# Kernel tuning notes

Hardware: AMD Instinct MI355X
Metric: run time of the kernel (lower is better)

Reference implementation:

```python
import jax, jax.numpy as jnp
import numpy as np
import math

B, QLEN, KLEN = 8, 128, 1024
KDIM = QDIM = ADIM = ODIM = 512
HM, HC = 4, 4            # monotonic / chunkwise heads
CHUNK = 4                # chunkwise attention window
EPS = 1e-6
SHARPENING = 1.0
NEG_INF = float(np.finfo(np.float32).min)


def moving_sum(x, back, forward):
    """Windowed sum over last axis: out[k] = sum_{j=k-back}^{k+forward} x[j].
    Equivalent to the conv1d-with-ones-filter moving_sum in the torch code."""
    K = x.shape[-1]
    xp = jnp.pad(x, [(0, 0)] * (x.ndim - 1) + [(back, forward)])
    cs = jnp.cumsum(xp, axis=-1)
    L = back + forward + 1
    upper = jax.lax.slice_in_dim(cs, L - 1, L - 1 + K, axis=-1)
    lower = jnp.concatenate([jnp.zeros_like(cs[..., :1]),
                             jax.lax.slice_in_dim(cs, 0, K - 1, axis=-1)], axis=-1)
    return upper - lower


def safe_cumprod(x, eps):
    """exp(exclusive_cumsum(log(clip(x, eps, 1)))) along last axis."""
    logx = jnp.log(jnp.clip(x, eps, 1.0))
    excl = jnp.concatenate([jnp.zeros_like(logx[..., :1]),
                            jnp.cumsum(logx, axis=-1)[..., :-1]], axis=-1)
    return jnp.exp(excl)


def _heads(x, w, b, h):
    y = x @ w + b                                   # [B, L, ADIM]
    bs, L, _ = y.shape
    return y.reshape(bs, L, h, -1).transpose(0, 2, 1, 3)  # [B, h, L, d_k]


def setup_inputs() -> dict:
    key = jax.random.key(0)
    ks = jax.random.split(key, 16)
    s = 0.02
    f32 = jnp.float32
    return {
        "key_x": jax.random.normal(ks[0], (B, KLEN, KDIM), f32),
        "query_x": jax.random.normal(ks[1], (B, QLEN, QDIM), f32),
        "mask": jnp.ones((B, QLEN, KLEN), jnp.int32),
        "wk_m": jax.random.normal(ks[2], (KDIM, ADIM), f32) * s,
        "bk_m": jnp.zeros((ADIM,), f32),
        "wq_m": jax.random.normal(ks[3], (QDIM, ADIM), f32) * s,
        "bq_m": jnp.zeros((ADIM,), f32),
        "r": jnp.asarray(-4.0, f32),
        "wk_c": jax.random.normal(ks[4], (KDIM, ADIM), f32) * s,
        "bk_c": jnp.zeros((ADIM,), f32),
        "wq_c": jax.random.normal(ks[5], (QDIM, ADIM), f32) * s,
        "bq_c": jnp.zeros((ADIM,), f32),
        "wv": jax.random.normal(ks[6], (KDIM, ADIM), f32) * s,
        "bv": jnp.zeros((ADIM,), f32),
        "wo": jax.random.normal(ks[7], (ADIM, ODIM), f32) * s,
        "bo": jnp.zeros((ODIM,), f32),
    }


def reference(key_x, query_x, mask, wk_m, bk_m, wq_m, bq_m, r,
              wk_c, bk_c, wq_c, bq_c, wv, bv, wo, bo):
    scale = math.sqrt(ADIM)
    m = (mask[:, None] > 0)                                    # [B,1,Q,K]

    # ---- monotonic energy (scaled_dot + offset r) ----
    km = _heads(key_x, wk_m, bk_m, HM)                         # [B,HM,K,dk]
    qm = _heads(query_x, wq_m, bq_m, HM)                       # [B,HM,Q,dk]
    e_mono = jnp.einsum('bhqd,bhkd->bhqk', qm, km) / scale + r
    e_mono = jnp.where(m, e_mono, NEG_INF)

    # ---- monotonic alpha via safe_cumprod + per-step cumsum recurrence ----
    p_choose = jax.nn.sigmoid(e_mono)                          # [B,HM,Q,K]
    cp = safe_cumprod(1.0 - p_choose, EPS)                     # [B,HM,Q,K]
    aw0 = jnp.zeros((B, HM, KLEN), e_mono.dtype).at[..., 0].set(1.0)

    def step(aw_prev, pc):
        p_i, cp_i = pc                                         # [B,HM,K]
        aw = p_i * cp_i * jnp.cumsum(aw_prev / jnp.maximum(cp_i, EPS), axis=-1)
        return aw, aw

    _, alpha = jax.lax.scan(step, aw0,
                            (p_choose.transpose(2, 0, 1, 3),
                             cp.transpose(2, 0, 1, 3)))
    alpha = alpha.transpose(1, 2, 0, 3)                        # [B,HM,Q,K]

    # ---- chunkwise energy ----
    kc = _heads(key_x, wk_c, bk_c, HC)
    qc = _heads(query_x, wq_c, bq_c, HC)
    e_chunk = jnp.einsum('bhqd,bhkd->bhqk', qc, kc) / scale
    e_chunk = jnp.where(m, e_chunk, NEG_INF)

    # ---- efficient chunkwise attention (clipped-logit trick) ----
    e = e_chunk - jnp.max(e_chunk, axis=-1, keepdims=True)
    sexp = jnp.maximum(jnp.exp(e), 1e-5)[:, None]              # [B,1,HC,Q,K]
    denom = moving_sum(sexp, CHUNK - 1, 0)                     # [B,1,HC,Q,K]
    beta = sexp * moving_sum(alpha[:, :, None] * SHARPENING / denom,
                             0, CHUNK - 1)                     # [B,HM,HC,Q,K]
    beta = beta.reshape(B, HM * HC, QLEN, KLEN)

    # ---- context + output projection ----
    v = (key_x @ wv + bv).reshape(B, KLEN, HM * HC, ADIM // (HM * HC))
    cv = jnp.einsum('bhqk,bkhd->bqhd', beta, v).reshape(B, QLEN, ADIM)
    return cv @ wo + bo
```

## Files before the change

kernel.cpp:

```cpp
#include <hip/hip_runtime.h>
#include <hip/hip_bf16.h>


#define NEG_INF (-3.402823466e38f)
#define EPS_MOCHA 1e-6f
#define INV_SCALE 0.04419417382415922f

typedef _Float16 half8 __attribute__((ext_vector_type(8)));
typedef _Float16 half4v __attribute__((ext_vector_type(4)));
typedef float f32x4 __attribute__((ext_vector_type(4)));

#define WAITBAR(N) asm volatile("s_waitcnt vmcnt(" #N ") lgkmcnt(0)\n\ts_barrier" ::: "memory")

__device__ __forceinline__ float wave_incl_scan(float x)
{
    int v;
    v = __builtin_amdgcn_update_dpp(0, __builtin_bit_cast(int, x), 0x111, 0xF, 0xF, false);
    x += __builtin_bit_cast(float, v);
    v = __builtin_amdgcn_update_dpp(0, __builtin_bit_cast(int, x), 0x112, 0xF, 0xF, false);
    x += __builtin_bit_cast(float, v);
    v = __builtin_amdgcn_update_dpp(0, __builtin_bit_cast(int, x), 0x114, 0xF, 0xF, false);
    x += __builtin_bit_cast(float, v);
    v = __builtin_amdgcn_update_dpp(0, __builtin_bit_cast(int, x), 0x118, 0xF, 0xF, false);
    x += __builtin_bit_cast(float, v);
    v = __builtin_amdgcn_update_dpp(0, __builtin_bit_cast(int, x), 0x142, 0xA, 0xF, false);
    x += __builtin_bit_cast(float, v);
    v = __builtin_amdgcn_update_dpp(0, __builtin_bit_cast(int, x), 0x143, 0xC, 0xF, false);
    x += __builtin_bit_cast(float, v);
    return x;
}

__global__ __launch_bounds__(256) void prep_weights(
    const float* __restrict__ wk_m, const float* __restrict__ wk_c,
    const float* __restrict__ wv, const float* __restrict__ wq_m,
    const float* __restrict__ wq_c, const float* __restrict__ wo,
    _Float16* __restrict__ Wt5, _Float16* __restrict__ Wt_wo)
{
    __shared__ float T[64][65];
    const int z = blockIdx.z;
    const float* W = (z == 0) ? wk_m : (z == 1) ? wk_c : (z == 2) ? wv
                   : (z == 3) ? wq_m : (z == 4) ? wq_c : wo;
    _Float16* O = (z < 5) ? (Wt5 + (size_t)z * 262144) : Wt_wo;
    const int n0 = blockIdx.x * 64, k0 = blockIdx.y * 64;
    const int t = threadIdx.x;
    const int rr = t >> 4, cc = (t & 15) * 4;
#pragma unroll
    for (int r = 0; r < 4; ++r) {
        int k = r * 16 + rr;
        float4 v = *(const float4*)(W + (size_t)(k0 + k) * 512 + n0 + cc);
        T[k][cc + 0] = v.x; T[k][cc + 1] = v.y;
        T[k][cc + 2] = v.z; T[k][cc + 3] = v.w;
    }
    __syncthreads();
    const int nn = t >> 2, kc = (t & 3) * 16;
    _Float16 tmp[16];
#pragma unroll
    for (int i = 0; i < 16; ++i) tmp[i] = (_Float16)T[kc + i][nn];
    _Float16* Op = O + (size_t)(n0 + nn) * 512 + k0 + kc;
    *(half8*)(Op)     = *(half8*)&tmp[0];
    *(half8*)(Op + 8) = *(half8*)&tmp[8];
}

__device__ __forceinline__ void mfma_step(half8 a[4], half8 b[4], f32x4 acc[4][4])
{
#pragma unroll
    for (int mt = 0; mt < 4; ++mt)
#pragma unroll
        for (int nt = 0; nt < 4; ++nt)
            acc[mt][nt] = __builtin_amdgcn_mfma_f32_16x16x32_f16(
                a[mt], b[nt], acc[mt][nt], 0, 0, 0);
}

__device__ __forceinline__ void stage16(const _Float16* src, _Float16* dst)
{
    __builtin_amdgcn_global_load_lds(
        (const __attribute__((address_space(1))) void*)src,
        (__attribute__((address_space(3))) void*)dst, 16, 0, 0);
}

__device__ __forceinline__ half8 cvt8(float4 a, float4 b)
{
    half8 h = {(_Float16)a.x, (_Float16)a.y, (_Float16)a.z, (_Float16)a.w,
               (_Float16)b.x, (_Float16)b.y, (_Float16)b.z, (_Float16)b.w};
    return h;
}

template <int NSTEPS>
__device__ __forceinline__ void gemm_acc_af32(
    const float* __restrict__ Abase, const _Float16* __restrict__ Bbase,
    _Float16* As, _Float16* Bs, f32x4 acc[4][4])
{
    const int tid = threadIdx.x;
    const int lane = tid & 63, wave = tid >> 6;
    const int wm = wave >> 1, wn = wave & 1;
    const int col = lane & 15, quad = lane >> 4;
    const int r0 = tid >> 2, seg = tid & 3;

    const float* Af0 = Abase + (size_t)r0 * 512 + seg * 8;
    const float* Af1 = Af0 + (size_t)64 * 512;
    const _Float16* Bg0 = Bbase + (size_t)r0 * 512 + seg * 8;
    const _Float16* Bg1 = Bg0 + (size_t)64 * 512;

    float4 pa0[2], pa1[2], pb0[2], pb1[2];

    pa0[0] = *(const float4*)(Af0);
    pa1[0] = *(const float4*)(Af0 + 4);
    pb0[0] = *(const float4*)(Af1);
    pb1[0] = *(const float4*)(Af1 + 4);
    stage16(Bg0, Bs + tid * 8);
    stage16(Bg1, Bs + 2048 + tid * 8);
    if (NSTEPS > 1) {
        stage16(Bg0 + 32, Bs + 4096 + tid * 8);
        stage16(Bg1 + 32, Bs + 4096 + 2048 + tid * 8);
    }
    *(half8*)(As + tid * 8)        = cvt8(pa0[0], pa1[0]);
    *(half8*)(As + 2048 + tid * 8) = cvt8(pb0[0], pb1[0]);
    if (NSTEPS > 1) {
        pa0[1] = *(const float4*)(Af0 + 32);
        pa1[1] = *(const float4*)(Af0 + 36);
        pb0[1] = *(const float4*)(Af1 + 32);
        pb1[1] = *(const float4*)(Af1 + 36);
    }
    if (NSTEPS > 1) WAITBAR(6);
    else            WAITBAR(0);

#pragma unroll
    for (int ks = 0; ks < NSTEPS; ++ks) {
        const int s = ks & 1;
        if (ks + 2 < NSTEPS) {
            const int k0 = (ks + 2) * 32;
            pa0[s] = *(const float4*)(Af0 + k0);
            pa1[s] = *(const float4*)(Af0 + k0 + 4);
            pb0[s] = *(const float4*)(Af1 + k0);
            pb1[s] = *(const float4*)(Af1 + k0 + 4);
        }
        if (ks + 2 < NSTEPS) {
            _Float16* Bbuf = Bs + ((ks + 2) % 3) * 4096;
            stage16(Bg0 + (ks + 2) * 32, Bbuf + tid * 8);
            stage16(Bg1 + (ks + 2) * 32, Bbuf + 2048 + tid * 8);
        }
        const _Float16* Afr = As + (ks & 1) * 4096 + (size_t)(wm * 64 + col) * 32 + quad * 8;
        const _Float16* Bfr = Bs + (ks % 3) * 4096 + (size_t)(wn * 64 + col) * 32 + quad * 8;
        half8 a[4], b[4];
#pragma unroll
        for (int t = 0; t < 4; ++t) {
            a[t] = *(const half8*)(Afr + (size_t)t * 16 * 32);
            b[t] = *(const half8*)(Bfr + (size_t)t * 16 * 32);
        }
        mfma_step(a, b, acc);
        if (ks + 1 < NSTEPS) {
            _Float16* Abuf = As + ((ks + 1) & 1) * 4096;
            *(half8*)(Abuf + tid * 8)        = cvt8(pa0[s ^ 1], pa1[s ^ 1]);
            *(half8*)(Abuf + 2048 + tid * 8) = cvt8(pb0[s ^ 1], pb1[s ^ 1]);
        }
        if (ks + 2 < NSTEPS)      WAITBAR(6);
        else if (ks + 1 < NSTEPS) WAITBAR(0);
    }
}

template <int NSTEPS>
__device__ __forceinline__ void gemm_acc_f16(
    const _Float16* __restrict__ Abase, const _Float16* __restrict__ Bbase,
    _Float16* As, _Float16* Bs, f32x4 acc[4][4])
{
    const int tid = threadIdx.x;
    const int lane = tid & 63, wave = tid >> 6;
    const int wm = wave >> 1, wn = wave & 1;
    const int col = lane & 15, quad = lane >> 4;
    const int r0 = tid >> 2, seg = tid & 3;

    const _Float16* Ag0 = Abase + (size_t)r0 * 512 + seg * 8;
    const _Float16* Ag1 = Ag0 + (size_t)64 * 512;
    const _Float16* Bg0 = Bbase + (size_t)r0 * 512 + seg * 8;
    const _Float16* Bg1 = Bg0 + (size_t)64 * 512;

    stage16(Ag0, As + tid * 8);
    stage16(Ag1, As + 2048 + tid * 8);
    stage16(Bg0, Bs + tid * 8);
    stage16(Bg1, Bs + 2048 + tid * 8);
    if (NSTEPS > 1) {
        stage16(Ag0 + 32, As + 4096 + tid * 8);
        stage16(Ag1 + 32, As + 4096 + 2048 + tid * 8);
        stage16(Bg0 + 32, Bs + 4096 + tid * 8);
        stage16(Bg1 + 32, Bs + 4096 + 2048 + tid * 8);
        WAITBAR(4);
    } else {
        WAITBAR(0);
    }

#pragma unroll
    for (int ks = 0; ks < NSTEPS; ++ks) {
        const int cur = ks % 3;
        if (ks + 2 < NSTEPS) {
            const int s2 = (ks + 2) % 3;
            stage16(Ag0 + (ks + 2) * 32, As + s2 * 4096 + tid * 8);
            stage16(Ag1 + (ks + 2) * 32, As + s2 * 4096 + 2048 + tid * 8);
            stage16(Bg0 + (ks + 2) * 32, Bs + s2 * 4096 + tid * 8);
            stage16(Bg1 + (ks + 2) * 32, Bs + s2 * 4096 + 2048 + tid * 8);
        }
        const _Float16* Afr = As + cur * 4096 + (size_t)(wm * 64 + col) * 32 + quad * 8;
        const _Float16* Bfr = Bs + cur * 4096 + (size_t)(wn * 64 + col) * 32 + quad * 8;
        half8 a[4], b[4];
#pragma unroll
        for (int t = 0; t < 4; ++t) {
            a[t] = *(const half8*)(Afr + (size_t)t * 16 * 32);
            b[t] = *(const half8*)(Bfr + (size_t)t * 16 * 32);
        }
        mfma_step(a, b, acc);
        if (ks + 2 < NSTEPS)      WAITBAR(4);
        else if (ks + 1 < NSTEPS) WAITBAR(0);
    }
}

__device__ __forceinline__ void proj_epilogue(
    f32x4 acc[4][4], const float* __restrict__ bias, void* __restrict__ Cv,
    int m0, int n0, int f16o)
{
    const int tid = threadIdx.x;
    const int lane = tid & 63, wave = tid >> 6;
    const int wm = wave >> 1, wn = wave & 1;
    const int col = lane & 15, quad = lane >> 4;
    float bnt[4];
#pragma unroll
    for (int nt = 0; nt < 4; ++nt)
        bnt[nt] = bias[n0 + wn * 64 + nt * 16 + col];
#pragma unroll
    for (int mt = 0; mt < 4; ++mt) {
        const int rowb = m0 + wm * 64 + mt * 16 + quad * 4;
#pragma unroll
        for (int nt = 0; nt < 4; ++nt) {
            const int cc = n0 + wn * 64 + nt * 16 + col;
#pragma unroll
            for (int r = 0; r < 4; ++r) {
                float v = acc[mt][nt][r] + bnt[nt];
                if (f16o)
                    ((_Float16*)Cv)[(size_t)(rowb + r) * 512 + cc] = (_Float16)v;
                else
                    ((float*)Cv)[(size_t)(rowb + r) * 512 + cc] = v;
            }
        }
    }
}

__global__ __launch_bounds__(256) void mfma_proj5(
    const float* __restrict__ key_x, const float* __restrict__ query_x,
    const _Float16* __restrict__ Wt5,
    const float* __restrict__ b0, void* __restrict__ C0,
    const float* __restrict__ b1, void* __restrict__ C1,
    const float* __restrict__ b2, void* __restrict__ C2,
    const float* __restrict__ b3, void* __restrict__ C3,
    const float* __restrict__ b4, void* __restrict__ C4)
{
    __shared__ _Float16 As[8192];
    __shared__ _Float16 Bs[12288];
    const int bid = (blockIdx.x & 7) * 104 + (blockIdx.x >> 3);
    int g, mblk, nblk;
    if (bid < 768) {
        g = bid >> 8; mblk = (bid & 255) >> 2; nblk = bid & 3;
    } else {
        const int t = bid - 768;
        g = 3 + (t >> 5); mblk = (t & 31) >> 2; nblk = t & 3;
    }
    const bool qry = g >= 3;
    const float* A = qry ? query_x : key_x;
    const _Float16* Wt = Wt5 + (size_t)g * 262144;
    const float* bias = (g == 0) ? b0 : (g == 1) ? b1 : (g == 2) ? b2
                      : (g == 3) ? b3 : b4;
    void* Cv = (g == 0) ? C0 : (g == 1) ? C1 : (g == 2) ? C2
             : (g == 3) ? C3 : C4;
    const int f16o = (g == 2) ? 0 : 1;
    const int m0 = mblk * 128, n0 = nblk * 128;

    f32x4 acc[4][4];
#pragma unroll
    for (int mt = 0; mt < 4; ++mt)
#pragma unroll
        for (int nt = 0; nt < 4; ++nt) acc[mt][nt] = (f32x4)0.f;
    gemm_acc_af32<16>(A + (size_t)m0 * 512, Wt + (size_t)n0 * 512, As, Bs, acc);
    proj_epilogue(acc, bias, Cv, m0, n0, f16o);
}

__global__ __launch_bounds__(256) void mfma_proj_out(
    const _Float16* __restrict__ A16, const _Float16* __restrict__ Wt,
    const float* __restrict__ bias, float* __restrict__ C)
{
    __shared__ _Float16 As[12288];
    __shared__ _Float16 Bs[12288];
    const int m0 = blockIdx.x * 128, n0 = blockIdx.y * 128;
    f32x4 acc[4][4];
#pragma unroll
    for (int mt = 0; mt < 4; ++mt)
#pragma unroll
        for (int nt = 0; nt < 4; ++nt) acc[mt][nt] = (f32x4)0.f;
    gemm_acc_f16<16>(A16 + (size_t)m0 * 512, Wt + (size_t)n0 * 512, As, Bs, acc);
    proj_epilogue(acc, bias, C, m0, n0, 0);
}

__global__ __launch_bounds__(256) void energy_mfma(
    const _Float16* __restrict__ Qm, const _Float16* __restrict__ Km,
    const _Float16* __restrict__ Qc, const _Float16* __restrict__ Kc,
    const int* __restrict__ mask, float* __restrict__ e_mono,
    _Float16* __restrict__ e_chunk16, const float* __restrict__ r_ptr)
{
    __shared__ _Float16 As[12288];
    __shared__ _Float16 Bs[12288];
    const int tid = threadIdx.x;
    const int lane = tid & 63, wave = tid >> 6;
    const int wm = wave >> 1, wn = wave & 1;
    const int col = lane & 15, quad = lane >> 4;
    const int kt0 = blockIdx.x * 128;
    const int h = blockIdx.y;
    const int b = blockIdx.z;
    const float rv = r_ptr[0];
    const int r0 = tid >> 2, seg = tid & 3;

    const _Float16* QmB = Qm + (size_t)(b * 128) * 512 + h * 128;
    const _Float16* QcB = Qc + (size_t)(b * 128) * 512 + h * 128;
    const _Float16* KmB = Km + (size_t)(b * 1024 + kt0) * 512 + h * 128;
    const _Float16* KcB = Kc + (size_t)(b * 1024 + kt0) * 512 + h * 128;
    const _Float16* Am0 = QmB + (size_t)r0 * 512 + seg * 8;
    const _Float16* Ac0 = QcB + (size_t)r0 * 512 + seg * 8;
    const _Float16* Bm0 = KmB + (size_t)r0 * 512 + seg * 8;
    const _Float16* Bc0 = KcB + (size_t)r0 * 512 + seg * 8;
#define EGA(s) (((s) < 4 ? Am0 : Ac0) + ((s) & 3) * 32)
#define EGB(s) (((s) < 4 ? Bm0 : Bc0) + ((s) & 3) * 32)

    f32x4 accM[4][4], accC[4][4];
#pragma unroll
    for (int mt = 0; mt < 4; ++mt)
#pragma unroll
        for (int nt = 0; nt < 4; ++nt) { accM[mt][nt] = (f32x4)0.f; accC[mt][nt] = (f32x4)0.f; }

#pragma unroll
    for (int s = 0; s < 2; ++s) {
        stage16(EGA(s), As + s * 4096 + tid * 8);
        stage16(EGA(s) + (size_t)64 * 512, As + s * 4096 + 2048 + tid * 8);
        stage16(EGB(s), Bs + s * 4096 + tid * 8);
        stage16(EGB(s) + (size_t)64 * 512, Bs + s * 4096 + 2048 + tid * 8);
    }
    WAITBAR(4);

#pragma unroll
    for (int ks = 0; ks < 8; ++ks) {
        const int cur = ks % 3;
        if (ks + 2 < 8) {
            const int s2 = (ks + 2) % 3;
            stage16(EGA(ks + 2), As + s2 * 4096 + tid * 8);
            stage16(EGA(ks + 2) + (size_t)64 * 512, As + s2 * 4096 + 2048 + tid * 8);
            stage16(EGB(ks + 2), Bs + s2 * 4096 + tid * 8);
            stage16(EGB(ks + 2) + (size_t)64 * 512, Bs + s2 * 4096 + 2048 + tid * 8);
        }
        const _Float16* Afr = As + cur * 4096 + (size_t)(wm * 64 + col) * 32 + quad * 8;
        const _Float16* Bfr = Bs + cur * 4096 + (size_t)(wn * 64 + col) * 32 + quad * 8;
        half8 a[4], bfr[4];
#pragma unroll
        for (int t = 0; t < 4; ++t) {
            a[t]   = *(const half8*)(Afr + (size_t)t * 16 * 32);
            bfr[t] = *(const half8*)(Bfr + (size_t)t * 16 * 32);
        }
        if (ks < 4) mfma_step(a, bfr, accM);
        else        mfma_step(a, bfr, accC);
        if (ks + 2 < 8)      WAITBAR(4);
        else if (ks + 1 < 8) WAITBAR(0);
    }
#undef EGA
#undef EGB

#pragma unroll
    for (int mt = 0; mt < 4; ++mt) {
        const int qb = wm * 64 + mt * 16 + quad * 4;
#pragma unroll
        for (int nt = 0; nt < 4; ++nt) {
            const int kc = kt0 + wn * 64 + nt * 16 + col;
#pragma unroll
            for (int r = 0; r < 4; ++r) {
                const int q = qb + r;
                const int mv = mask[((size_t)b * 128 + q) * 1024 + kc];
                const size_t oi = (((size_t)b * 4 + h) * 128 + q) * 1024 + kc;
                float vm = accM[mt][nt][r] * INV_SCALE + rv;
                e_mono[oi] = mv ? vm : NEG_INF;
                float vc = accC[mt][nt][r] * INV_SCALE;
                e_chunk16[oi] = (_Float16)(mv ? vc : NEG_INF);
            }
        }
    }
}

__device__ __forceinline__ void transcend_row(
    const float* __restrict__ Erow, int lane, float o_pcp[16], float o_inv[16])
{
    const float* E = Erow + lane * 16;
    float e[16];
    *(float4*)&e[0]  = *(const float4*)(E);
    *(float4*)&e[4]  = *(const float4*)(E + 4);
    *(float4*)&e[8]  = *(const float4*)(E + 8);
    *(float4*)&e[12] = *(const float4*)(E + 12);

    float p[16], l[16];
#pragma unroll
    for (int i = 0; i < 16; ++i) {
        p[i] = 1.f / (1.f + expf(-e[i]));
        l[i] = logf(fmaxf(1.f - p[i], EPS_MOCHA));
    }
    float incl[16];
    incl[0] = l[0];
#pragma unroll
    for (int i = 1; i < 16; ++i) incl[i] = incl[i - 1] + l[i];
    float total = incl[15];
    float x = wave_incl_scan(total);
    float base = x - total;
#pragma unroll
    for (int i = 0; i < 16; ++i) {
        float cl = base + (i ? incl[i - 1] : 0.f);
        float cp = expf(cl);
        o_pcp[i] = p[i] * cp;
        o_inv[i] = 1.f / fmaxf(cp, EPS_MOCHA);
    }
}

#define SW2(k) ((k) + ((k) >> 4))

__global__ __launch_bounds__(256) void alpha_pre(
    const float* __restrict__ e_mono, float* __restrict__ G,
    float* __restrict__ pcp)
{
    __shared__ float pshare[4][1088];
    const int tid = threadIdx.x;
    const int lane = tid & 63;
    const int wid = tid >> 6;
    const int row = blockIdx.x * 4 + wid;
    const int q = row & 127;

    float pq[16], iq[16];
    transcend_row(e_mono + (size_t)row * 1024, lane, pq, iq);

    float* P = pcp + (size_t)row * 1024 + lane * 16;
    *(float4*)(P)      = *(float4*)&pq[0];
    *(float4*)(P + 4)  = *(float4*)&pq[4];
    *(float4*)(P + 8)  = *(float4*)&pq[8];
    *(float4*)(P + 12) = *(float4*)&pq[12];

#pragma unroll
    for (int i = 0; i < 16; ++i)
        pshare[wid][SW2(lane * 16 + i)] = pq[i];
    __syncthreads();

    float g[16];
    if (q == 0) {
#pragma unroll
        for (int i = 0; i < 16; ++i) g[i] = 0.f;
        if (lane == 0) g[0] = iq[0];
    } else if (wid > 0) {
#pragma unroll
        for (int i = 0; i < 16; ++i)
            g[i] = pshare[wid - 1][SW2(lane * 16 + i)] * iq[i];
    } else {
        float pm[16], im[16];
        transcend_row(e_mono + (size_t)(row - 1) * 1024, lane, pm, im);
#pragma unroll
        for (int i = 0; i < 16; ++i) g[i] = pm[i] * iq[i];
    }
    float* Gp = G + (size_t)row * 1024 + lane * 16;
    *(float4*)(Gp)      = *(float4*)&g[0];
    *(float4*)(Gp + 4)  = *(float4*)&g[4];
    *(float4*)(Gp + 8)  = *(float4*)&g[8];
    *(float4*)(Gp + 12) = *(float4*)&g[12];
}

__global__ __launch_bounds__(64, 1) void alpha_scan(
    const float* __restrict__ G, float* __restrict__ S)
{
    const int lane = threadIdx.x;
    const int bh = blockIdx.x;
    const float* Gp = G + (size_t)bh * 131072 + lane * 16;
    float* Sp = S + (size_t)bh * 131072 + lane * 16;

    float bg[8][16];
#pragma unroll
    for (int s = 0; s < 8; ++s) {
        const float* Gq = Gp + (size_t)s * 1024;
        *(float4*)&bg[s][0]  = *(const float4*)(Gq);
        *(float4*)&bg[s][4]  = *(const float4*)(Gq + 4);
        *(float4*)&bg[s][8]  = *(const float4*)(Gq + 8);
        *(float4*)&bg[s][12] = *(const float4*)(Gq + 12);
    }

    float Sv[16];
#pragma unroll
    for (int i = 0; i < 16; ++i) Sv[i] = 1.f;

    for (int q8 = 0; q8 < 128; q8 += 8) {
#pragma unroll
        for (int s = 0; s < 8; ++s) {
            const int q = q8 + s;
            float g[16];
#pragma unroll
            for (int i = 0; i < 16; ++i) g[i] = bg[s][i];
            if (q + 8 < 128) {
                const float* Gq = Gp + (size_t)(q + 8) * 1024;
                *(float4*)&bg[s][0]  = *(const float4*)(Gq);
                *(float4*)&bg[s][4]  = *(const float4*)(Gq + 4);
                *(float4*)&bg[s][8]  = *(const float4*)(Gq + 8);
                *(float4*)&bg[s][12] = *(const float4*)(Gq + 12);
            }

            float incl[16];
            incl[0] = g[0] * Sv[0];
#pragma unroll
            for (int i = 1; i < 16; ++i)
                incl[i] = fmaf(g[i], Sv[i], incl[i - 1]);
            float total = incl[15];
            float x = wave_incl_scan(total);
            float base = x - total;
#pragma unroll
            for (int i = 0; i < 16; ++i) Sv[i] = base + incl[i];

            float* Sq = Sp + (size_t)q * 1024;
            *(float4*)(Sq)      = *(float4*)&Sv[0];
            *(float4*)(Sq + 4)  = *(float4*)&Sv[4];
            *(float4*)(Sq + 8)  = *(float4*)&Sv[8];
            *(float4*)(Sq + 12) = *(float4*)&Sv[12];
        }
    }
}

__global__ __launch_bounds__(256) void beta_kernel(
    const _Float16* __restrict__ e_chunk16, const float* __restrict__ pcp,
    const float* __restrict__ S, _Float16* __restrict__ beta)
{
    __shared__ float red[4];
    __shared__ float edge_sx[4][4];
    __shared__ float edge_t[4][4][4];
    const int q = blockIdx.x, b = blockIdx.y;
    const int tid = threadIdx.x;
    const int lane = tid & 63, wid = tid >> 6;
    const int k4 = tid * 4;

    float av[4][4];
#pragma unroll
    for (int hm = 0; hm < 4; ++hm) {
        const size_t off = (((size_t)b * 4 + hm) * 128 + q) * 1024 + k4;
        float4 pv = *(const float4*)(pcp + off);
        float4 sv = *(const float4*)(S + off);
        av[hm][0] = pv.x * sv.x;
        av[hm][1] = pv.y * sv.y;
        av[hm][2] = pv.z * sv.z;
        av[hm][3] = pv.w * sv.w;
    }

    for (int hc = 0; hc < 4; ++hc) {
        half4v ev = *(const half4v*)(e_chunk16 + (((size_t)b * 4 + hc) * 128 + q) * 1024 + k4);
        float e[4] = {(float)ev[0], (float)ev[1], (float)ev[2], (float)ev[3]};

        float mx = fmaxf(fmaxf(e[0], e[1]), fmaxf(e[2], e[3]));
#pragma unroll
        for (int off = 32; off >= 1; off >>= 1)
            mx = fmaxf(mx, __shfl_xor(mx, off, 64));
        if (lane == 0) red[wid] = mx;
        __syncthreads();
        mx = fmaxf(fmaxf(red[0], red[1]), fmaxf(red[2], red[3]));

        float sx[4];
#pragma unroll
        for (int i = 0; i < 4; ++i)
            sx[i] = fmaxf(expf(e[i] - mx), 1e-5f);
        if (lane == 63) {
            edge_sx[wid][0] = sx[0]; edge_sx[wid][1] = sx[1];
            edge_sx[wid][2] = sx[2]; edge_sx[wid][3] = sx[3];
        }
        __syncthreads();

        float p1 = __shfl_up(sx[3], 1, 64);
        float p2 = __shfl_up(sx[2], 1, 64);
        float p3 = __shfl_up(sx[1], 1, 64);
        if (lane == 0) {
            if (wid > 0) {
                p1 = edge_sx[wid - 1][3];
                p2 = edge_sx[wid - 1][2];
                p3 = edge_sx[wid - 1][1];
            } else {
                p1 = 0.f; p2 = 0.f; p3 = 0.f;
            }
        }
        float den[4];
        den[0] = sx[0] + p1 + p2 + p3;
        den[1] = sx[1] + sx[0] + p1 + p2;
        den[2] = sx[2] + sx[1] + sx[0] + p1;
        den[3] = sx[3] + sx[2] + sx[1] + sx[0];

        float t[4][4];
#pragma unroll
        for (int hm = 0; hm < 4; ++hm)
#pragma unroll
            for (int i = 0; i < 4; ++i)
                t[hm][i] = av[hm][i] / den[i];
        if (lane == 0) {
#pragma unroll
            for (int hm = 0; hm < 4; ++hm) {
                edge_t[wid][hm][0] = t[hm][0]; edge_t[wid][hm][1] = t[hm][1];
                edge_t[wid][hm][2] = t[hm][2]; edge_t[wid][hm][3] = t[hm][3];
            }
        }
        __syncthreads();

#pragma unroll
        for (int hm = 0; hm < 4; ++hm) {
            float n1 = __shfl_down(t[hm][0], 1, 64);
            float n2 = __shfl_down(t[hm][1], 1, 64);
            float n3 = __shfl_down(t[hm][2], 1, 64);
            if (lane == 63) {
                if (wid < 3) {
                    n1 = edge_t[wid + 1][hm][0];
                    n2 = edge_t[wid + 1][hm][1];
                    n3 = edge_t[wid + 1][hm][2];
                } else {
                    n1 = 0.f; n2 = 0.f; n3 = 0.f;
                }
            }
            float o0 = sx[0] * (t[hm][0] + t[hm][1] + t[hm][2] + t[hm][3]);
            float o1 = sx[1] * (t[hm][1] + t[hm][2] + t[hm][3] + n1);
            float o2 = sx[2] * (t[hm][2] + t[hm][3] + n1 + n2);
            float o3 = sx[3] * (t[hm][3] + n1 + n2 + n3);
            _Float16* Brow = beta + (((size_t)b * 16 + hm * 4 + hc) * 128 + q) * 1024;
            half4v hv = {(_Float16)o0, (_Float16)o1, (_Float16)o2, (_Float16)o3};
            *(half4v*)(Brow + k4) = hv;
        }
    }
}

__global__ __launch_bounds__(256) void context_kernel(
    const _Float16* __restrict__ beta, const float* __restrict__ V,
    _Float16* __restrict__ cv16)
{
    __shared__ float bS[128][64];
    __shared__ float vS[128][32];
    const int qh = blockIdx.x, h = blockIdx.y, b = blockIdx.z;
    const int tid = threadIdx.x;
    const int ty = tid >> 3, tx = tid & 7;
    const int q0 = qh * 64;

    const _Float16* Bbase = beta + (((size_t)b * 16 + h) * 128 + q0) * 1024;
    const float* Vbase = V + (size_t)b * 1024 * 512 + h * 32;

    float acc[2][4];
#pragma unroll
    for (int i = 0; i < 2; ++i)
#pragma unroll
        for (int j = 0; j < 4; ++j) acc[i][j] = 0.f;

    for (int k0 = 0; k0 < 1024; k0 += 128) {
        {
            int r = tid >> 2, c = tid & 3;
#pragma unroll
            for (int s = 0; s < 4; ++s) {
                half8 v = *(const half8*)(Bbase + (size_t)r * 1024 + k0 + s * 32 + c * 8);
#pragma unroll
                for (int j = 0; j < 8; ++j) bS[s * 32 + c * 8 + j][r] = (float)v[j];
            }
        }
        {
            int kk = tid >> 3, c = tid & 7;
#pragma unroll
            for (int s = 0; s < 4; ++s) {
                float4 v = *(const float4*)(Vbase + (size_t)(k0 + s * 32 + kk) * 512 + c * 4);
                *(float4*)&vS[s * 32 + kk][c * 4] = v;
            }
        }
        __syncthreads();
#pragma unroll 8
        for (int kk = 0; kk < 128; ++kk) {
            float a0 = bS[kk][ty * 2], a1 = bS[kk][ty * 2 + 1];
            float bb[4];
            *(float4*)bb = *(const float4*)&vS[kk][tx * 4];
#pragma unroll
            for (int j = 0; j < 4; ++j) {
                acc[0][j] = fmaf(a0, bb[j], acc[0][j]);
                acc[1][j] = fmaf(a1, bb[j], acc[1][j]);
            }
        }
        __syncthreads();
    }
#pragma unroll
    for (int i = 0; i < 2; ++i) {
        _Float16* Cp = cv16 + ((size_t)b * 128 + q0 + ty * 2 + i) * 512 + h * 32 + tx * 4;
        half4v hv = {(_Float16)acc[i][0], (_Float16)acc[i][1],
                     (_Float16)acc[i][2], (_Float16)acc[i][3]};
        *(half4v*)Cp = hv;
    }
}

extern "C" void kernel_launch(void* const* d_in, const int* in_sizes, int n_in,
                              void* d_out, int out_size, void* d_ws, size_t ws_size,
                              hipStream_t stream)
{
    const float* key_x   = (const float*)d_in[0];
    const float* query_x = (const float*)d_in[1];
    const int*   mask    = (const int*)d_in[2];
    const float* wk_m = (const float*)d_in[3];
    const float* bk_m = (const float*)d_in[4];
    const float* wq_m = (const float*)d_in[5];
    const float* bq_m = (const float*)d_in[6];
    const float* r    = (const float*)d_in[7];
    const float* wk_c = (const float*)d_in[8];
    const float* bk_c = (const float*)d_in[9];
    const float* wq_c = (const float*)d_in[10];
    const float* bq_c = (const float*)d_in[11];
    const float* wv   = (const float*)d_in[12];
    const float* bv   = (const float*)d_in[13];
    const float* wo   = (const float*)d_in[14];
    const float* bo   = (const float*)d_in[15];
    float* out = (float*)d_out;

    float* ws = (float*)d_ws;
    _Float16* hws = (_Float16*)d_ws;
    const size_t MEGF = 1024 * 1024;
    _Float16* Km16  = hws;
    _Float16* Kc16  = hws + 4 * MEGF;
    _Float16* Qm16  = hws + 8 * MEGF;
    _Float16* Qc16  = hws + 8 * MEGF + 524288;
    float* e_mono  = ws + 11 * MEGF;
    _Float16* e_chunk16 = hws + 34 * MEGF;
    float* V       = ws + 19 * MEGF;
    float* G       = ws;
    float* pcp     = ws + 4 * MEGF;
    float* S       = ws + 23 * MEGF;
    _Float16* beta16 = hws + 16 * MEGF;
    _Float16* Wt5   = hws + 54 * MEGF;
    _Float16* Wt_wo = hws + 54 * MEGF + 5 * 262144;
    _Float16* cv16  = hws + 55 * MEGF + MEGF / 2;

    prep_weights<<<dim3(8, 8, 6), 256, 0, stream>>>(
        wk_m, wk_c, wv, wq_m, wq_c, wo, Wt5, Wt_wo);
    mfma_proj5<<<dim3(832), 256, 0, stream>>>(
        key_x, query_x, Wt5,
        bk_m, Km16, bk_c, Kc16, bv, V, bq_m, Qm16, bq_c, Qc16);
    energy_mfma<<<dim3(8, 4, 8), 256, 0, stream>>>(
        Qm16, Km16, Qc16, Kc16, mask, e_mono, e_chunk16, r);
    alpha_pre<<<dim3(1024), 256, 0, stream>>>(e_mono, G, pcp);
    alpha_scan<<<dim3(32), 64, 0, stream>>>(G, S);
    beta_kernel<<<dim3(128, 8), 256, 0, stream>>>(e_chunk16, pcp, S, beta16);
    context_kernel<<<dim3(2, 16, 8), 256, 0, stream>>>(beta16, V, cv16);
    mfma_proj_out<<<dim3(8, 4), 256, 0, stream>>>(cv16, Wt_wo, bo, out);
}
```

Before: 256.8 us.

## Pre-convert activations to fp16 and use 512-thread 8-wave GEMM blocks

Adds a separate kernel that converts key_x and query_x to fp16 up front, so the projection GEMM can stage both operands through direct global-to-LDS loads. The projection, energy and output GEMMs move from 256-thread blocks (4 waves, 4x4 MFMA tiles each) to 512-thread blocks (8 waves, 4x2 tiles each). This halves per-wave accumulator registers and raises wave count per block to improve latency hiding. It costs an extra kernel launch plus a full fp16 write and re-read of the activations, and each wave now does less work per LDS fragment load.

```diff
diff --git a/kernel.cpp b/kernel.cpp
--- a/kernel.cpp
+++ b/kernel.cpp
@@ -30,6 +30,25 @@
     return x;
 }
 
+__device__ __forceinline__ half8 cvt8(float4 a, float4 b)
+{
+    half8 h = {(_Float16)a.x, (_Float16)a.y, (_Float16)a.z, (_Float16)a.w,
+               (_Float16)b.x, (_Float16)b.y, (_Float16)b.z, (_Float16)b.w};
+    return h;
+}
+
+__global__ __launch_bounds__(256) void cvt_x(
+    const float* __restrict__ key_x, const float* __restrict__ query_x,
+    _Float16* __restrict__ X16)
+{
+    const size_t KELEMS = (size_t)8192 * 512;
+    size_t o = ((size_t)blockIdx.x * 256 + threadIdx.x) * 8;
+    const float* s = (o < KELEMS) ? (key_x + o) : (query_x + (o - KELEMS));
+    float4 a = *(const float4*)s;
+    float4 b = *(const float4*)(s + 4);
+    *(half8*)(X16 + o) = cvt8(a, b);
+}
+
 __global__ __launch_bounds__(256) void prep_weights(
     const float* __restrict__ wk_m, const float* __restrict__ wk_c,
     const float* __restrict__ wv, const float* __restrict__ wq_m,
@@ -61,16 +80,6 @@
     *(half8*)(Op + 8) = *(half8*)&tmp[8];
 }
 
-__device__ __forceinline__ void mfma_step(half8 a[4], half8 b[4], f32x4 acc[4][4])
-{
-#pragma unroll
-    for (int mt = 0; mt < 4; ++mt)
-#pragma unroll
-        for (int nt = 0; nt < 4; ++nt)
-            acc[mt][nt] = __builtin_amdgcn_mfma_f32_16x16x32_f16(
-                a[mt], b[nt], acc[mt][nt], 0, 0, 0);
-}
-
 __device__ __forceinline__ void stage16(const _Float16* src, _Float16* dst)
 {
     __builtin_amdgcn_global_load_lds(
@@ -78,112 +87,26 @@
         (__attribute__((address_space(3))) void*)dst, 16, 0, 0);
 }
 
-__device__ __forceinline__ half8 cvt8(float4 a, float4 b)
-{
-    half8 h = {(_Float16)a.x, (_Float16)a.y, (_Float16)a.z, (_Float16)a.w,
-               (_Float16)b.x, (_Float16)b.y, (_Float16)b.z, (_Float16)b.w};
-    return h;
-}
-
 template <int NSTEPS>
-__device__ __forceinline__ void gemm_acc_af32(
-    const float* __restrict__ Abase, const _Float16* __restrict__ Bbase,
-    _Float16* As, _Float16* Bs, f32x4 acc[4][4])
+__device__ __forceinline__ void gemm8_f16(
+    const _Float16* __restrict__ Abase, const _Float16* __restrict__ Bbase,
+    _Float16* As, _Float16* Bs, f32x4 acc[4][2])
 {
     const int tid = threadIdx.x;
     const int lane = tid & 63, wave = tid >> 6;
-    const int wm = wave >> 1, wn = wave & 1;
+    const int wm = wave >> 2, wn = wave & 3;
     const int col = lane & 15, quad = lane >> 4;
     const int r0 = tid >> 2, seg = tid & 3;
 
-    const float* Af0 = Abase + (size_t)r0 * 512 + seg * 8;
-    const float* Af1 = Af0 + (size_t)64 * 512;
-    const _Float16* Bg0 = Bbase + (size_t)r0 * 512 + seg * 8;
-    const _Float16* Bg1 = Bg0 + (size_t)64 * 512;
-
-    float4 pa0[2], pa1[2], pb0[2], pb1[2];
-
-    pa0[0] = *(const float4*)(Af0);
-    pa1[0] = *(const float4*)(Af0 + 4);
-    pb0[0] = *(const float4*)(Af1);
-    pb1[0] = *(const float4*)(Af1 + 4);
-    stage16(Bg0, Bs + tid * 8);
-    stage16(Bg1, Bs + 2048 + tid * 8);
+    const _Float16* Ag = Abase + (size_t)r0 * 512 + seg * 8;
+    const _Float16* Bg = Bbase + (size_t)r0 * 512 + seg * 8;
+
+    stage16(Ag, As + tid * 8);
+    stage16(Bg, Bs + tid * 8);
     if (NSTEPS > 1) {
-        stage16(Bg0 + 32, Bs + 4096 + tid * 8);
-        stage16(Bg1 + 32, Bs + 4096 + 2048 + tid * 8);
-    }
-    *(half8*)(As + tid * 8)        = cvt8(pa0[0], pa1[0]);
-    *(half8*)(As + 2048 + tid * 8) = cvt8(pb0[0], pb1[0]);
-    if (NSTEPS > 1) {
-        pa0[1] = *(const float4*)(Af0 + 32);
-        pa1[1] = *(const float4*)(Af0 + 36);
-        pb0[1] = *(const float4*)(Af1 + 32);
-        pb1[1] = *(const float4*)(Af1 + 36);
-    }
-    if (NSTEPS > 1) WAITBAR(6);
-    else            WAITBAR(0);
-
-#pragma unroll
-    for (int ks = 0; ks < NSTEPS; ++ks) {
-        const int s = ks & 1;
-        if (ks + 2 < NSTEPS) {
-            const int k0 = (ks + 2) * 32;
-            pa0[s] = *(const float4*)(Af0 + k0);
-            pa1[s] = *(const float4*)(Af0 + k0 + 4);
-            pb0[s] = *(const float4*)(Af1 + k0);
-            pb1[s] = *(const float4*)(Af1 + k0 + 4);
-        }
-        if (ks + 2 < NSTEPS) {
-            _Float16* Bbuf = Bs + ((ks + 2) % 3) * 4096;
-            stage16(Bg0 + (ks + 2) * 32, Bbuf + tid * 8);
-            stage16(Bg1 + (ks + 2) * 32, Bbuf + 2048 + tid * 8);
-        }
-        const _Float16* Afr = As + (ks & 1) * 4096 + (size_t)(wm * 64 + col) * 32 + quad * 8;
-        const _Float16* Bfr = Bs + (ks % 3) * 4096 + (size_t)(wn * 64 + col) * 32 + quad * 8;
-        half8 a[4], b[4];
-#pragma unroll
-        for (int t = 0; t < 4; ++t) {
-            a[t] = *(const half8*)(Afr + (size_t)t * 16 * 32);
-            b[t] = *(const half8*)(Bfr + (size_t)t * 16 * 32);
-        }
-        mfma_step(a, b, acc);
-        if (ks + 1 < NSTEPS) {
-            _Float16* Abuf = As + ((ks + 1) & 1) * 4096;
-            *(half8*)(Abuf + tid * 8)        = cvt8(pa0[s ^ 1], pa1[s ^ 1]);
-            *(half8*)(Abuf + 2048 + tid * 8) = cvt8(pb0[s ^ 1], pb1[s ^ 1]);
-        }
-        if (ks + 2 < NSTEPS)      WAITBAR(6);
-        else if (ks + 1 < NSTEPS) WAITBAR(0);
-    }
-}
-
-template <int NSTEPS>
-__device__ __forceinline__ void gemm_acc_f16(
-    const _Float16* __restrict__ Abase, const _Float16* __restrict__ Bbase,
-    _Float16* As, _Float16* Bs, f32x4 acc[4][4])
-{
-    const int tid = threadIdx.x;
-    const int lane = tid & 63, wave = tid >> 6;
-    const int wm = wave >> 1, wn = wave & 1;
-    const int col = lane & 15, quad = lane >> 4;
-    const int r0 = tid >> 2, seg = tid & 3;
-
-    const _Float16* Ag0 = Abase + (size_t)r0 * 512 + seg * 8;
-    const _Float16* Ag1 = Ag0 + (size_t)64 * 512;
-    const _Float16* Bg0 = Bbase + (size_t)r0 * 512 + seg * 8;
-    const _Float16* Bg1 = Bg0 + (size_t)64 * 512;
-
-    stage16(Ag0, As + tid * 8);
-    stage16(Ag1, As + 2048 + tid * 8);
-    stage16(Bg0, Bs + tid * 8);
-    stage16(Bg1, Bs + 2048 + tid * 8);
-    if (NSTEPS > 1) {
-        stage16(Ag0 + 32, As + 4096 + tid * 8);
-        stage16(Ag1 + 32, As + 4096 + 2048 + tid * 8);
-        stage16(Bg0 + 32, Bs + 4096 + tid * 8);
-        stage16(Bg1 + 32, Bs + 4096 + 2048 + tid * 8);
-        WAITBAR(4);
+        stage16(Ag + 32, As + 4096 + tid * 8);
+        stage16(Bg + 32, Bs + 4096 + tid * 8);
+        WAITBAR(2);
     } else {
         WAITBAR(0);
     }
@@ -193,43 +116,45 @@
         const int cur = ks % 3;
         if (ks + 2 < NSTEPS) {
             const int s2 = (ks + 2) % 3;
-            stage16(Ag0 + (ks + 2) * 32, As + s2 * 4096 + tid * 8);
-            stage16(Ag1 + (ks + 2) * 32, As + s2 * 4096 + 2048 + tid * 8);
-            stage16(Bg0 + (ks + 2) * 32, Bs + s2 * 4096 + tid * 8);
-            stage16(Bg1 + (ks + 2) * 32, Bs + s2 * 4096 + 2048 + tid * 8);
+            stage16(Ag + (ks + 2) * 32, As + s2 * 4096 + tid * 8);
+            stage16(Bg + (ks + 2) * 32, Bs + s2 * 4096 + tid * 8);
         }
         const _Float16* Afr = As + cur * 4096 + (size_t)(wm * 64 + col) * 32 + quad * 8;
-        const _Float16* Bfr = Bs + cur * 4096 + (size_t)(wn * 64 + col) * 32 + quad * 8;
-        half8 a[4], b[4];
-#pragma unroll
-        for (int t = 0; t < 4; ++t) {
-            a[t] = *(const half8*)(Afr + (size_t)t * 16 * 32);
-            b[t] = *(const half8*)(Bfr + (size_t)t * 16 * 32);
-        }
-        mfma_step(a, b, acc);
-        if (ks + 2 < NSTEPS)      WAITBAR(4);
+        const _Float16* Bfr = Bs + cur * 4096 + (size_t)(wn * 32 + col) * 32 + quad * 8;
+        half8 a[4], b[2];
+#pragma unroll
+        for (int t = 0; t < 4; ++t) a[t] = *(const half8*)(Afr + (size_t)t * 16 * 32);
+#pragma unroll
+        for (int t = 0; t < 2; ++t) b[t] = *(const half8*)(Bfr + (size_t)t * 16 * 32);
+#pragma unroll
+        for (int mt = 0; mt < 4; ++mt)
+#pragma unroll
+            for (int nt = 0; nt < 2; ++nt)
+                acc[mt][nt] = __builtin_amdgcn_mfma_f32_16x16x32_f16(
+                    a[mt], b[nt], acc[mt][nt], 0, 0, 0);
+        if (ks + 2 < NSTEPS)      WAITBAR(2);
         else if (ks + 1 < NSTEPS) WAITBAR(0);
     }
 }
 
-__device__ __forceinline__ void proj_epilogue(
-    f32x4 acc[4][4], const float* __restrict__ bias, void* __restrict__ Cv,
+__device__ __forceinline__ void proj_epilogue8(
+    f32x4 acc[4][2], const float* __restrict__ bias, void* __restrict__ Cv,
     int m0, int n0, int f16o)
 {
     const int tid = threadIdx.x;
     const int lane = tid & 63, wave = tid >> 6;
-    const int wm = wave >> 1, wn = wave & 1;
+    const int wm = wave >> 2, wn = wave & 3;
     const int col = lane & 15, quad = lane >> 4;
-    float bnt[4];
-#pragma unroll
-    for (int nt = 0; nt < 4; ++nt)
-        bnt[nt] = bias[n0 + wn * 64 + nt * 16 + col];
+    float bnt[2];
+#pragma unroll
+    for (int nt = 0; nt < 2; ++nt)
+        bnt[nt] = bias[n0 + wn * 32 + nt * 16 + col];
 #pragma unroll
     for (int mt = 0; mt < 4; ++mt) {
         const int rowb = m0 + wm * 64 + mt * 16 + quad * 4;
 #pragma unroll
-        for (int nt = 0; nt < 4; ++nt) {
-            const int cc = n0 + wn * 64 + nt * 16 + col;
+        for (int nt = 0; nt < 2; ++nt) {
+            const int cc = n0 + wn * 32 + nt * 16 + col;
 #pragma unroll
             for (int r = 0; r < 4; ++r) {
                 float v = acc[mt][nt][r] + bnt[nt];
@@ -242,16 +167,15 @@
     }
 }
 
-__global__ __launch_bounds__(256) void mfma_proj5(
-    const float* __restrict__ key_x, const float* __restrict__ query_x,
-    const _Float16* __restrict__ Wt5,
+__global__ __launch_bounds__(512, 8) void mfma_proj5(
+    const _Float16* __restrict__ X16, const _Float16* __restrict__ Wt5,
     const float* __restrict__ b0, void* __restrict__ C0,
     const float* __restrict__ b1, void* __restrict__ C1,
     const float* __restrict__ b2, void* __restrict__ C2,
     const float* __restrict__ b3, void* __restrict__ C3,
     const float* __restrict__ b4, void* __restrict__ C4)
 {
-    __shared__ _Float16 As[8192];
+    __shared__ _Float16 As[12288];
     __shared__ _Float16 Bs[12288];
     const int bid = (blockIdx.x & 7) * 104 + (blockIdx.x >> 3);
     int g, mblk, nblk;
@@ -262,7 +186,7 @@
         g = 3 + (t >> 5); mblk = (t & 31) >> 2; nblk = t & 3;
     }
     const bool qry = g >= 3;
-    const float* A = qry ? query_x : key_x;
+    const _Float16* A = X16 + (qry ? (size_t)8192 * 512 : 0);
     const _Float16* Wt = Wt5 + (size_t)g * 262144;
     const float* bias = (g == 0) ? b0 : (g == 1) ? b1 : (g == 2) ? b2
                       : (g == 3) ? b3 : b4;
@@ -271,32 +195,32 @@
     const int f16o = (g == 2) ? 0 : 1;
     const int m0 = mblk * 128, n0 = nblk * 128;
 
-    f32x4 acc[4][4];
+    f32x4 acc[4][2];
 #pragma unroll
     for (int mt = 0; mt < 4; ++mt)
 #pragma unroll
-        for (int nt = 0; nt < 4; ++nt) acc[mt][nt] = (f32x4)0.f;
-    gemm_acc_af32<16>(A + (size_t)m0 * 512, Wt + (size_t)n0 * 512, As, Bs, acc);
-    proj_epilogue(acc, bias, Cv, m0, n0, f16o);
-}
-
-__global__ __launch_bounds__(256) void mfma_proj_out(
+        for (int nt = 0; nt < 2; ++nt) acc[mt][nt] = (f32x4)0.f;
+    gemm8_f16<16>(A + (size_t)m0 * 512, Wt + (size_t)n0 * 512, As, Bs, acc);
+    proj_epilogue8(acc, bias, Cv, m0, n0, f16o);
+}
+
+__global__ __launch_bounds__(512, 4) void mfma_proj_out(
     const _Float16* __restrict__ A16, const _Float16* __restrict__ Wt,
     const float* __restrict__ bias, float* __restrict__ C)
 {
     __shared__ _Float16 As[12288];
     __shared__ _Float16 Bs[12288];
     const int m0 = blockIdx.x * 128, n0 = blockIdx.y * 128;
-    f32x4 acc[4][4];
+    f32x4 acc[4][2];
 #pragma unroll
     for (int mt = 0; mt < 4; ++mt)
 #pragma unroll
-        for (int nt = 0; nt < 4; ++nt) acc[mt][nt] = (f32x4)0.f;
-    gemm_acc_f16<16>(A16 + (size_t)m0 * 512, Wt + (size_t)n0 * 512, As, Bs, acc);
-    proj_epilogue(acc, bias, C, m0, n0, 0);
-}
-
-__global__ __launch_bounds__(256) void energy_mfma(
+        for (int nt = 0; nt < 2; ++nt) acc[mt][nt] = (f32x4)0.f;
+    gemm8_f16<16>(A16 + (size_t)m0 * 512, Wt + (size_t)n0 * 512, As, Bs, acc);
+    proj_epilogue8(acc, bias, C, m0, n0, 0);
+}
+
+__global__ __launch_bounds__(512, 4) void energy_mfma(
     const _Float16* __restrict__ Qm, const _Float16* __restrict__ Km,
     const _Float16* __restrict__ Qc, const _Float16* __restrict__ Kc,
     const int* __restrict__ mask, float* __restrict__ e_mono,
@@ -306,7 +230,7 @@
     __shared__ _Float16 Bs[12288];
     const int tid = threadIdx.x;
     const int lane = tid & 63, wave = tid >> 6;
-    const int wm = wave >> 1, wn = wave & 1;
+    const int wm = wave >> 2, wn = wave & 3;
     const int col = lane & 15, quad = lane >> 4;
     const int kt0 = blockIdx.x * 128;
     const int h = blockIdx.y;
@@ -314,31 +238,25 @@
     const float rv = r_ptr[0];
     const int r0 = tid >> 2, seg = tid & 3;
 
-    const _Float16* QmB = Qm + (size_t)(b * 128) * 512 + h * 128;
-    const _Float16* QcB = Qc + (size_t)(b * 128) * 512 + h * 128;
-    const _Float16* KmB = Km + (size_t)(b * 1024 + kt0) * 512 + h * 128;
-    const _Float16* KcB = Kc + (size_t)(b * 1024 + kt0) * 512 + h * 128;
-    const _Float16* Am0 = QmB + (size_t)r0 * 512 + seg * 8;
-    const _Float16* Ac0 = QcB + (size_t)r0 * 512 + seg * 8;
-    const _Float16* Bm0 = KmB + (size_t)r0 * 512 + seg * 8;
-    const _Float16* Bc0 = KcB + (size_t)r0 * 512 + seg * 8;
+    const _Float16* Am0 = Qm + (size_t)(b * 128) * 512 + h * 128 + (size_t)r0 * 512 + seg * 8;
+    const _Float16* Ac0 = Qc + (size_t)(b * 128) * 512 + h * 128 + (size_t)r0 * 512 + seg * 8;
+    const _Float16* Bm0 = Km + (size_t)(b * 1024 + kt0) * 512 + h * 128 + (size_t)r0 * 512 + seg * 8;
+    const _Float16* Bc0 = Kc + (size_t)(b * 1024 + kt0) * 512 + h * 128 + (size_t)r0 * 512 + seg * 8;
 #define EGA(s) (((s) < 4 ? Am0 : Ac0) + ((s) & 3) * 32)
 #define EGB(s) (((s) < 4 ? Bm0 : Bc0) + ((s) & 3) * 32)
 
-    f32x4 accM[4][4], accC[4][4];
+    f32x4 accM[4][2], accC[4][2];
 #pragma unroll
     for (int mt = 0; mt < 4; ++mt)
 #pragma unroll
-        for (int nt = 0; nt < 4; ++nt) { accM[mt][nt] = (f32x4)0.f; accC[mt][nt] = (f32x4)0.f; }
+        for (int nt = 0; nt < 2; ++nt) { accM[mt][nt] = (f32x4)0.f; accC[mt][nt] = (f32x4)0.f; }
 
 #pragma unroll
     for (int s = 0; s < 2; ++s) {
         stage16(EGA(s), As + s * 4096 + tid * 8);
-        stage16(EGA(s) + (size_t)64 * 512, As + s * 4096 + 2048 + tid * 8);
         stage16(EGB(s), Bs + s * 4096 + tid * 8);
-        stage16(EGB(s) + (size_t)64 * 512, Bs + s * 4096 + 2048 + tid * 8);
-    }
-    WAITBAR(4);
+    }
+    WAITBAR(2);
 
 #pragma unroll
     for (int ks = 0; ks < 8; ++ks) {
@@ -346,21 +264,29 @@
         if (ks + 2 < 8) {
             const int s2 = (ks + 2) % 3;
             stage16(EGA(ks + 2), As + s2 * 4096 + tid * 8);
-            stage16(EGA(ks + 2) + (size_t)64 * 512, As + s2 * 4096 + 2048 + tid * 8);
             stage16(EGB(ks + 2), Bs + s2 * 4096 + tid * 8);
-            stage16(EGB(ks + 2) + (size_t)64 * 512, Bs + s2 * 4096 + 2048 + tid * 8);
         }
         const _Float16* Afr = As + cur * 4096 + (size_t)(wm * 64 + col) * 32 + quad * 8;
-        const _Float16* Bfr = Bs + cur * 4096 + (size_t)(wn * 64 + col) * 32 + quad * 8;
-        half8 a[4], bfr[4];
-#pragma unroll
-        for (int t = 0; t < 4; ++t) {
-            a[t]   = *(const half8*)(Afr + (size_t)t * 16 * 32);
-            bfr[t] = *(const half8*)(Bfr + (size_t)t * 16 * 32);
-        }
-        if (ks < 4) mfma_step(a, bfr, accM);
-        else        mfma_step(a, bfr, accC);
-        if (ks + 2 < 8)      WAITBAR(4);
+        const _Float16* Bfr = Bs + cur * 4096 + (size_t)(wn * 32 + col) * 32 + quad * 8;
+        half8 a[4], bf[2];
+#pragma unroll
+        for (int t = 0; t < 4; ++t) a[t]  = *(const half8*)(Afr + (size_t)t * 16 * 32);
+#pragma unroll
+        for (int t = 0; t < 2; ++t) bf[t] = *(const half8*)(Bfr + (size_t)t * 16 * 32);
+        if (ks < 4) {
+#pragma unroll
+            for (int mt = 0; mt < 4; ++mt)
+#pragma unroll
+                for (int nt = 0; nt < 2; ++nt)
+                    accM[mt][nt] = __builtin_amdgcn_mfma_f32_16x16x32_f16(a[mt], bf[nt], accM[mt][nt], 0, 0, 0);
+        } else {
+#pragma unroll
+            for (int mt = 0; mt < 4; ++mt)
+#pragma unroll
+                for (int nt = 0; nt < 2; ++nt)
+                    accC[mt][nt] = __builtin_amdgcn_mfma_f32_16x16x32_f16(a[mt], bf[nt], accC[mt][nt], 0, 0, 0);
+        }
+        if (ks + 2 < 8)      WAITBAR(2);
         else if (ks + 1 < 8) WAITBAR(0);
     }
 #undef EGA
@@ -370,8 +296,8 @@
     for (int mt = 0; mt < 4; ++mt) {
         const int qb = wm * 64 + mt * 16 + quad * 4;
 #pragma unroll
-        for (int nt = 0; nt < 4; ++nt) {
-            const int kc = kt0 + wn * 64 + nt * 16 + col;
+        for (int nt = 0; nt < 2; ++nt) {
+            const int kc = kt0 + wn * 32 + nt * 16 + col;
 #pragma unroll
             for (int r = 0; r < 4; ++r) {
                 const int q = qb + r;
@@ -718,6 +644,7 @@
     _Float16* Kc16  = hws + 4 * MEGF;
     _Float16* Qm16  = hws + 8 * MEGF;
     _Float16* Qc16  = hws + 8 * MEGF + 524288;
+    _Float16* X16   = hws + 16 * MEGF;
     float* e_mono  = ws + 11 * MEGF;
     _Float16* e_chunk16 = hws + 34 * MEGF;
     float* V       = ws + 19 * MEGF;
@@ -729,16 +656,16 @@
     _Float16* Wt_wo = hws + 54 * MEGF + 5 * 262144;
     _Float16* cv16  = hws + 55 * MEGF + MEGF / 2;
 
+    cvt_x<<<dim3(2304), 256, 0, stream>>>(key_x, query_x, X16);
     prep_weights<<<dim3(8, 8, 6), 256, 0, stream>>>(
         wk_m, wk_c, wv, wq_m, wq_c, wo, Wt5, Wt_wo);
-    mfma_proj5<<<dim3(832), 256, 0, stream>>>(
-        key_x, query_x, Wt5,
-        bk_m, Km16, bk_c, Kc16, bv, V, bq_m, Qm16, bq_c, Qc16);
-    energy_mfma<<<dim3(8, 4, 8), 256, 0, stream>>>(
+    mfma_proj5<<<dim3(832), 512, 0, stream>>>(
+        X16, Wt5, bk_m, Km16, bk_c, Kc16, bv, V, bq_m, Qm16, bq_c, Qc16);
+    energy_mfma<<<dim3(8, 4, 8), 512, 0, stream>>>(
         Qm16, Km16, Qc16, Kc16, mask, e_mono, e_chunk16, r);
     alpha_pre<<<dim3(1024), 256, 0, stream>>>(e_mono, G, pcp);
     alpha_scan<<<dim3(32), 64, 0, stream>>>(G, S);
     beta_kernel<<<dim3(128, 8), 256, 0, stream>>>(e_chunk16, pcp, S, beta16);
     context_kernel<<<dim3(2, 16, 8), 256, 0, stream>>>(beta16, V, cv16);
-    mfma_proj_out<<<dim3(8, 4), 256, 0, stream>>>(cv16, Wt_wo, bo, out);
-}
+    mfma_proj_out<<<dim3(8, 4), 512, 0, stream>>>(cv16, Wt_wo, bo, out);
+}
```

Result: no change. 252.4 us (-1.7%).
